# Performance work log

Measured on AMD Instinct MI355X. Metric: run time of the kernel, lower is better.

## Reference

```python
import jax, jax.numpy as jnp
import numpy as np

DIM = 2048
BATCH = 16384


def setup_inputs() -> dict:
    key = jax.random.key(0)
    k_x, k_h, k_w, k_b, k_d = jax.random.split(key, 5)
    x = jax.random.normal(k_x, (BATCH, DIM), dtype=jnp.float32)
    h = jax.random.normal(k_h, (BATCH, DIM), dtype=jnp.float32)
    # nn.Linear(dim, dim): weight [out, in], bias [out]
    W = jax.random.normal(k_w, (DIM, DIM), dtype=jnp.float32) / np.sqrt(DIM)
    b = jax.random.normal(k_b, (DIM,), dtype=jnp.float32) * 0.01
    # nn.Parameter(torch.zeros(dim)) initialized to zeros, but use small random for nontrivial grads
    decay = jax.random.normal(k_d, (DIM,), dtype=jnp.float32) * 0.1
    return {"x": x, "h": h, "W": W, "b": b, "decay": decay}


def reference(x, h, W, b, decay):
    # alpha = sigmoid(decay); h_new = alpha * h + x @ W^T + b
    alpha = jax.nn.sigmoid(decay)  # [dim]
    h_new = alpha * h + jnp.einsum("bd,ed->be", x, W) + b  # [batch, dim]
    return (h_new, h_new)
```

## Files before the change

kernel.cpp:

```cpp
#include <hip/hip_runtime.h>
#include <hip/hip_bf16.h>

#define M_BATCH 16384
#define N_DIM   2048
#define K_DIM   2048

typedef __attribute__((ext_vector_type(8))) short bf16x8;
typedef __attribute__((ext_vector_type(4))) float f32x4;

__device__ __forceinline__ unsigned short f2bf_rne(float f) {
    union { float f; unsigned int u; } v; v.f = f;
    unsigned int r = v.u + 0x7fffu + ((v.u >> 16) & 1u);
    return (unsigned short)(r >> 16);
}

__global__ __launch_bounds__(256) void cvt_f32_bf16_x8(
        const float* __restrict__ src, unsigned short* __restrict__ dst, int n8) {
    int i = blockIdx.x * blockDim.x + threadIdx.x;
    if (i >= n8) return;
    const float4* s4 = (const float4*)src;
    float4 a = s4[2 * i];
    float4 b = s4[2 * i + 1];
    union { unsigned short h[8]; uint4 v; } r;
    r.h[0] = f2bf_rne(a.x); r.h[1] = f2bf_rne(a.y);
    r.h[2] = f2bf_rne(a.z); r.h[3] = f2bf_rne(a.w);
    r.h[4] = f2bf_rne(b.x); r.h[5] = f2bf_rne(b.y);
    r.h[6] = f2bf_rne(b.z); r.h[7] = f2bf_rne(b.w);
    ((uint4*)dst)[i] = r.v;
}

__device__ __forceinline__ void gld_lds16(const void* g, void* l) {
    __builtin_amdgcn_global_load_lds(
        (const __attribute__((address_space(1))) void*)g,
        (__attribute__((address_space(3))) void*)l, 16, 0, 0);
}

__global__ __launch_bounds__(256, 2) void lrnn_gemm_fused(
        const unsigned short* __restrict__ Xb,
        const unsigned short* __restrict__ Wb,
        const float* __restrict__ H,
        const float* __restrict__ bias,
        const float* __restrict__ decay,
        float* __restrict__ out) {
    __shared__ __align__(16) unsigned short As[128 * 32];
    __shared__ __align__(16) unsigned short Bs[128 * 32];

    const int tid  = threadIdx.x;
    const int wave = tid >> 6;
    const int lane = tid & 63;
    const int quad = lane >> 4;
    const int l16  = lane & 15;

    const int row0 = blockIdx.y * 128;
    const int col0 = blockIdx.x * 128;
    const int wm = (wave >> 1) * 64;
    const int wn = (wave & 1) * 64;

    const int t0  = wave * 64 + lane;
    const int r0s = t0 >> 2, kc0 = (t0 & 3) * 8;
    const int t1  = 256 + t0;
    const int r1s = t1 >> 2, kc1 = (t1 & 3) * 8;

    const unsigned short* gA0 = Xb + (size_t)(row0 + r0s) * K_DIM + kc0;
    const unsigned short* gA1 = Xb + (size_t)(row0 + r1s) * K_DIM + kc1;
    const unsigned short* gB0 = Wb + (size_t)(col0 + r0s) * K_DIM + kc0;
    const unsigned short* gB1 = Wb + (size_t)(col0 + r1s) * K_DIM + kc1;

    unsigned short* lA0 = As + (wave * 64) * 8;
    unsigned short* lA1 = As + (256 + wave * 64) * 8;
    unsigned short* lB0 = Bs + (wave * 64) * 8;
    unsigned short* lB1 = Bs + (256 + wave * 64) * 8;

    f32x4 acc[4][4] = {};

    for (int k0 = 0; k0 < K_DIM; k0 += 32) {
        gld_lds16(gA0 + k0, lA0);
        gld_lds16(gA1 + k0, lA1);
        gld_lds16(gB0 + k0, lB0);
        gld_lds16(gB1 + k0, lB1);
        __syncthreads();

        bf16x8 af[4], bfr[4];
#pragma unroll
        for (int i = 0; i < 4; ++i) {
            af[i]  = *(const bf16x8*)(As + (wm + i * 16 + l16) * 32 + quad * 8);
            bfr[i] = *(const bf16x8*)(Bs + (wn + i * 16 + l16) * 32 + quad * 8);
        }
#pragma unroll
        for (int i = 0; i < 4; ++i)
#pragma unroll
            for (int j = 0; j < 4; ++j)
                acc[i][j] = __builtin_amdgcn_mfma_f32_16x16x32_bf16(
                    af[i], bfr[j], acc[i][j], 0, 0, 0);
        __syncthreads();
    }

    const size_t MN = (size_t)M_BATCH * N_DIM;
#pragma unroll
    for (int j = 0; j < 4; ++j) {
        const int col = col0 + wn + j * 16 + l16;
        const float al = 1.0f / (1.0f + __expf(-decay[col]));
        const float bb = bias[col];
#pragma unroll
        for (int i = 0; i < 4; ++i) {
            const int row = row0 + wm + i * 16 + quad * 4;
#pragma unroll
            for (int r = 0; r < 4; ++r) {
                size_t idx = (size_t)(row + r) * N_DIM + col;
                float v = al * H[idx] + acc[i][j][r] + bb;
                out[idx] = v;
                out[MN + idx] = v;
            }
        }
    }
}

extern "C" void kernel_launch(void* const* d_in, const int* in_sizes, int n_in,
                              void* d_out, int out_size, void* d_ws, size_t ws_size,
                              hipStream_t stream) {
    const float* x     = (const float*)d_in[0];
    const float* h     = (const float*)d_in[1];
    const float* W     = (const float*)d_in[2];
    const float* b     = (const float*)d_in[3];
    const float* decay = (const float*)d_in[4];
    float* out = (float*)d_out;

    unsigned short* xb = (unsigned short*)d_ws;
    unsigned short* wb = xb + (size_t)M_BATCH * K_DIM;

    const int n8x = M_BATCH * K_DIM / 8;
    cvt_f32_bf16_x8<<<n8x / 256, 256, 0, stream>>>(x, xb, n8x);
    const int n8w = N_DIM * K_DIM / 8;
    cvt_f32_bf16_x8<<<n8w / 256, 256, 0, stream>>>(W, wb, n8w);

    dim3 grid(N_DIM / 128, M_BATCH / 128);
    lrnn_gemm_fused<<<grid, 256, 0, stream>>>(xb, wb, h, b, decay, out);
}
```

Baseline: 612.1 us.

## Rewrite GEMM as 256x256 tile, 8-wave, double-buffered swizzled LDS pipeline

Result: slower. 681.6 us (+11.4%).

```diff
diff --git a/kernel.cpp b/kernel.cpp
--- a/kernel.cpp
+++ b/kernel.cpp
@@ -1,5 +1,4 @@
 #include <hip/hip_runtime.h>
-#include <hip/hip_bf16.h>
 
 #define M_BATCH 16384
 #define N_DIM   2048
@@ -29,81 +28,158 @@
     ((uint4*)dst)[i] = r.v;
 }
 
-__device__ __forceinline__ void gld_lds16(const void* g, void* l) {
+__device__ __forceinline__ void gld_lds16(const unsigned short* g, unsigned short* l) {
     __builtin_amdgcn_global_load_lds(
         (const __attribute__((address_space(1))) void*)g,
         (__attribute__((address_space(3))) void*)l, 16, 0, 0);
 }
 
-__global__ __launch_bounds__(256, 2) void lrnn_gemm_fused(
+#define BAR()   __builtin_amdgcn_s_barrier()
+#define LGKM0() asm volatile("s_waitcnt lgkmcnt(0)" ::: "memory")
+#define VMC4()  asm volatile("s_waitcnt vmcnt(4)" ::: "memory")
+#define PRIO1() __builtin_amdgcn_s_setprio(1)
+#define PRIO0() __builtin_amdgcn_s_setprio(0)
+
+__global__ __launch_bounds__(512, 2) void lrnn_gemm_fused(
         const unsigned short* __restrict__ Xb,
         const unsigned short* __restrict__ Wb,
         const float* __restrict__ H,
         const float* __restrict__ bias,
         const float* __restrict__ decay,
         float* __restrict__ out) {
-    __shared__ __align__(16) unsigned short As[128 * 32];
-    __shared__ __align__(16) unsigned short Bs[128 * 32];
+    extern __shared__ char smem_raw[];
+    unsigned short* lds = (unsigned short*)smem_raw;
 
     const int tid  = threadIdx.x;
     const int wave = tid >> 6;
     const int lane = tid & 63;
-    const int quad = lane >> 4;
     const int l16  = lane & 15;
-
-    const int row0 = blockIdx.y * 128;
-    const int col0 = blockIdx.x * 128;
-    const int wm = (wave >> 1) * 64;
-    const int wn = (wave & 1) * 64;
-
-    const int t0  = wave * 64 + lane;
-    const int r0s = t0 >> 2, kc0 = (t0 & 3) * 8;
-    const int t1  = 256 + t0;
-    const int r1s = t1 >> 2, kc1 = (t1 & 3) * 8;
-
-    const unsigned short* gA0 = Xb + (size_t)(row0 + r0s) * K_DIM + kc0;
-    const unsigned short* gA1 = Xb + (size_t)(row0 + r1s) * K_DIM + kc1;
-    const unsigned short* gB0 = Wb + (size_t)(col0 + r0s) * K_DIM + kc0;
-    const unsigned short* gB1 = Wb + (size_t)(col0 + r1s) * K_DIM + kc1;
-
-    unsigned short* lA0 = As + (wave * 64) * 8;
-    unsigned short* lA1 = As + (256 + wave * 64) * 8;
-    unsigned short* lB0 = Bs + (wave * 64) * 8;
-    unsigned short* lB1 = Bs + (256 + wave * 64) * 8;
-
-    f32x4 acc[4][4] = {};
-
-    for (int k0 = 0; k0 < K_DIM; k0 += 32) {
-        gld_lds16(gA0 + k0, lA0);
-        gld_lds16(gA1 + k0, lA1);
-        gld_lds16(gB0 + k0, lB0);
-        gld_lds16(gB1 + k0, lB1);
-        __syncthreads();
-
-        bf16x8 af[4], bfr[4];
-#pragma unroll
-        for (int i = 0; i < 4; ++i) {
-            af[i]  = *(const bf16x8*)(As + (wm + i * 16 + l16) * 32 + quad * 8);
-            bfr[i] = *(const bf16x8*)(Bs + (wn + i * 16 + l16) * 32 + quad * 8);
-        }
-#pragma unroll
-        for (int i = 0; i < 4; ++i)
-#pragma unroll
-            for (int j = 0; j < 4; ++j)
-                acc[i][j] = __builtin_amdgcn_mfma_f32_16x16x32_bf16(
-                    af[i], bfr[j], acc[i][j], 0, 0, 0);
-        __syncthreads();
+    const int q    = lane >> 4;
+    const int l7   = lane & 7;
+    const int wm   = wave >> 2;
+    const int wn   = wave & 3;
+
+    const int row0 = blockIdx.y * 256;
+    const int col0 = blockIdx.x * 256;
+
+    const int r0c = tid >> 3,      s0c = (tid & 7) ^ (r0c & 7);
+    const int c1  = 512 + tid;
+    const int r1c = c1 >> 3,       s1c = (c1 & 7) ^ (r1c & 7);
+    const size_t off0 = (size_t)r0c * K_DIM + s0c * 8;
+    const size_t off1 = (size_t)r1c * K_DIM + s1c * 8;
+    const int stl0 = wave * 512;
+    const int stl1 = 4096 + wave * 512;
+
+    const unsigned short* Xg = Xb + (size_t)row0 * K_DIM;
+    const unsigned short* Wg = Wb + (size_t)col0 * K_DIM;
+    const size_t hstride = (size_t)128 * K_DIM;
+
+    int roF[4][2];
+#pragma unroll
+    for (int i_ = 0; i_ < 4; ++i_)
+#pragma unroll
+        for (int k_ = 0; k_ < 2; ++k_)
+            roF[i_][k_] = (i_ * 16 + l16) * 64 + (((q + 4 * k_) ^ l7) * 8);
+
+    const unsigned short* rdA = lds + wm * 8192;
+    const unsigned short* rdB = lds + 16384 + (wn >> 1) * 8192 + (wn & 1) * 4096;
+
+    f32x4 acc[8][4] = {};
+    bf16x8 a[4][2], b[2][2];
+
+#define STAGE_A(buf, h, t) do { \
+    unsigned short* lb_ = lds + (buf) * 32768 + (h) * 8192; \
+    const unsigned short* gs_ = Xg + (size_t)(h) * hstride + (size_t)(t) * 64; \
+    gld_lds16(gs_ + off0, lb_ + stl0); \
+    gld_lds16(gs_ + off1, lb_ + stl1); } while (0)
+
+#define STAGE_B(buf, h, t) do { \
+    unsigned short* lb_ = lds + (buf) * 32768 + 16384 + (h) * 8192; \
+    const unsigned short* gs_ = Wg + (size_t)(h) * hstride + (size_t)(t) * 64; \
+    gld_lds16(gs_ + off0, lb_ + stl0); \
+    gld_lds16(gs_ + off1, lb_ + stl1); } while (0)
+
+#define LOAD_A(buf, qi) do { \
+    const unsigned short* p_ = rdA + (buf) * 32768 + (qi) * 4096; \
+    _Pragma("unroll") for (int i_ = 0; i_ < 4; ++i_) \
+    _Pragma("unroll") for (int k_ = 0; k_ < 2; ++k_) \
+        a[i_][k_] = *(const bf16x8*)(p_ + roF[i_][k_]); } while (0)
+
+#define LOAD_B(buf, qj) do { \
+    const unsigned short* p_ = rdB + (buf) * 32768 + (qj) * 2048; \
+    _Pragma("unroll") for (int j_ = 0; j_ < 2; ++j_) \
+    _Pragma("unroll") for (int k_ = 0; k_ < 2; ++k_) \
+        b[j_][k_] = *(const bf16x8*)(p_ + roF[j_][k_]); } while (0)
+
+#define MFMA_Q(qi, qj) do { \
+    _Pragma("unroll") for (int i_ = 0; i_ < 4; ++i_) \
+    _Pragma("unroll") for (int j_ = 0; j_ < 2; ++j_) \
+    _Pragma("unroll") for (int k_ = 0; k_ < 2; ++k_) \
+        acc[(qi)*4 + i_][(qj)*2 + j_] = __builtin_amdgcn_mfma_f32_16x16x32_bf16( \
+            a[i_][k_], b[j_][k_], acc[(qi)*4 + i_][(qj)*2 + j_], 0, 0, 0); } while (0)
+
+    STAGE_A(0, 0, 0); STAGE_A(0, 1, 0); STAGE_B(0, 0, 0); STAGE_B(0, 1, 0);
+    STAGE_A(1, 0, 1); STAGE_A(1, 1, 1);
+    VMC4();
+    BAR();
+
+#pragma unroll 1
+    for (int it = 0; it < 16; ++it) {
+        const int t1 = 2 * it + 1;
+        const int u0 = (2 * it + 2) & 31;
+        const int u1 = (2 * it + 3) & 31;
+
+        LOAD_A(0, 0); LOAD_B(0, 0);
+        STAGE_B(1, 0, t1); STAGE_B(1, 1, t1);
+        BAR(); LGKM0();
+        PRIO1(); MFMA_Q(0, 0); PRIO0();
+        BAR();
+        LOAD_B(0, 1);
+        BAR(); LGKM0();
+        PRIO1(); MFMA_Q(0, 1); PRIO0();
+        BAR();
+        LOAD_A(0, 1);
+        BAR(); LGKM0();
+        PRIO1(); MFMA_Q(1, 1); PRIO0();
+        BAR();
+        LOAD_B(0, 0);
+        STAGE_A(0, 0, u0); STAGE_A(0, 1, u0);
+        VMC4();
+        BAR(); LGKM0();
+        PRIO1(); MFMA_Q(1, 0); PRIO0();
+        BAR();
+        LOAD_A(1, 0); LOAD_B(1, 0);
+        STAGE_B(0, 0, u0); STAGE_B(0, 1, u0);
+        BAR(); LGKM0();
+        PRIO1(); MFMA_Q(0, 0); PRIO0();
+        BAR();
+        LOAD_B(1, 1);
+        BAR(); LGKM0();
+        PRIO1(); MFMA_Q(0, 1); PRIO0();
+        BAR();
+        LOAD_A(1, 1);
+        BAR(); LGKM0();
+        PRIO1(); MFMA_Q(1, 1); PRIO0();
+        BAR();
+        LOAD_B(1, 0);
+        STAGE_A(1, 0, u1); STAGE_A(1, 1, u1);
+        VMC4();
+        BAR(); LGKM0();
+        PRIO1(); MFMA_Q(1, 0); PRIO0();
+        BAR();
     }
 
+    asm volatile("s_waitcnt vmcnt(0)" ::: "memory");
+
     const size_t MN = (size_t)M_BATCH * N_DIM;
 #pragma unroll
     for (int j = 0; j < 4; ++j) {
-        const int col = col0 + wn + j * 16 + l16;
+        const int col = col0 + wn * 64 + j * 16 + l16;
         const float al = 1.0f / (1.0f + __expf(-decay[col]));
         const float bb = bias[col];
 #pragma unroll
-        for (int i = 0; i < 4; ++i) {
-            const int row = row0 + wm + i * 16 + quad * 4;
+        for (int i = 0; i < 8; ++i) {
+            const int row = row0 + wm * 128 + i * 16 + q * 4;
 #pragma unroll
             for (int r = 0; r < 4; ++r) {
                 size_t idx = (size_t)(row + r) * N_DIM + col;
@@ -113,6 +189,12 @@
             }
         }
     }
+
+#undef STAGE_A
+#undef STAGE_B
+#undef LOAD_A
+#undef LOAD_B
+#undef MFMA_Q
 }
 
 extern "C" void kernel_launch(void* const* d_in, const int* in_sizes, int n_in,
@@ -128,11 +210,18 @@
     unsigned short* xb = (unsigned short*)d_ws;
     unsigned short* wb = xb + (size_t)M_BATCH * K_DIM;
 
+    static bool cfg = false;
+    if (!cfg) {
+        hipFuncSetAttribute((const void*)lrnn_gemm_fused,
+                            hipFuncAttributeMaxDynamicSharedMemorySize, 131072);
+        cfg = true;
+    }
+
     const int n8x = M_BATCH * K_DIM / 8;
     cvt_f32_bf16_x8<<<n8x / 256, 256, 0, stream>>>(x, xb, n8x);
     const int n8w = N_DIM * K_DIM / 8;
     cvt_f32_bf16_x8<<<n8w / 256, 256, 0, stream>>>(W, wb, n8w);
 
-    dim3 grid(N_DIM / 128, M_BATCH / 128);
-    lrnn_gemm_fused<<<grid, 256, 0, stream>>>(xb, wb, h, b, decay, out);
-}
+    dim3 grid(N_DIM / 256, M_BATCH / 256);
+    lrnn_gemm_fused<<<grid, 512, 131072, stream>>>(xb, wb, h, b, decay, out);
+}
```

## Double-buffer LDS with K=64 stages, XOR swizzle, and grouped tile remap

Applied to the files above, without the earlier changes.

Result: faster. 597.9 us (-2.3%).

```diff
diff --git a/kernel.cpp b/kernel.cpp
--- a/kernel.cpp
+++ b/kernel.cpp
@@ -1,5 +1,4 @@
 #include <hip/hip_runtime.h>
-#include <hip/hip_bf16.h>
 
 #define M_BATCH 16384
 #define N_DIM   2048
@@ -29,11 +28,17 @@
     ((uint4*)dst)[i] = r.v;
 }
 
-__device__ __forceinline__ void gld_lds16(const void* g, void* l) {
+__device__ __forceinline__ void gld_lds16(const unsigned short* g, unsigned short* l) {
     __builtin_amdgcn_global_load_lds(
         (const __attribute__((address_space(1))) void*)g,
         (__attribute__((address_space(3))) void*)l, 16, 0, 0);
 }
+
+#define BAR()   __builtin_amdgcn_s_barrier()
+#define LGKM0() asm volatile("s_waitcnt lgkmcnt(0)" ::: "memory")
+#define VMC0()  asm volatile("s_waitcnt vmcnt(0)" ::: "memory")
+#define PRIO1() __builtin_amdgcn_s_setprio(1)
+#define PRIO0() __builtin_amdgcn_s_setprio(0)
 
 __global__ __launch_bounds__(256, 2) void lrnn_gemm_fused(
         const unsigned short* __restrict__ Xb,
@@ -42,68 +47,104 @@
         const float* __restrict__ bias,
         const float* __restrict__ decay,
         float* __restrict__ out) {
-    __shared__ __align__(16) unsigned short As[128 * 32];
-    __shared__ __align__(16) unsigned short Bs[128 * 32];
+    __shared__ __align__(16) unsigned short lds[32768];
 
     const int tid  = threadIdx.x;
     const int wave = tid >> 6;
     const int lane = tid & 63;
-    const int quad = lane >> 4;
     const int l16  = lane & 15;
+    const int q    = lane >> 4;
+    const int l7   = lane & 7;
+    const int wr   = wave >> 1;
+    const int wc   = wave & 1;
 
-    const int row0 = blockIdx.y * 128;
-    const int col0 = blockIdx.x * 128;
-    const int wm = (wave >> 1) * 64;
-    const int wn = (wave & 1) * 64;
+    const int wid = blockIdx.y * 16 + blockIdx.x;
+    const int nid = (wid & 7) * 256 + (wid >> 3);
+    const int bx  = nid & 15;
+    const int by  = nid >> 4;
+    const int row0 = by * 128;
+    const int col0 = bx * 128;
 
-    const int t0  = wave * 64 + lane;
-    const int r0s = t0 >> 2, kc0 = (t0 & 3) * 8;
-    const int t1  = 256 + t0;
-    const int r1s = t1 >> 2, kc1 = (t1 & 3) * 8;
+    const unsigned short* gA[4];
+    const unsigned short* gB[4];
+    int ldst[4];
+#pragma unroll
+    for (int i = 0; i < 4; ++i) {
+        const int c = tid + 256 * i;
+        const int r = c >> 3;
+        const int s = (c & 7) ^ (r & 7);
+        gA[i] = Xb + (size_t)(row0 + r) * K_DIM + s * 8;
+        gB[i] = Wb + (size_t)(col0 + r) * K_DIM + s * 8;
+        ldst[i] = wave * 512 + i * 2048;
+    }
 
-    const unsigned short* gA0 = Xb + (size_t)(row0 + r0s) * K_DIM + kc0;
-    const unsigned short* gA1 = Xb + (size_t)(row0 + r1s) * K_DIM + kc1;
-    const unsigned short* gB0 = Wb + (size_t)(col0 + r0s) * K_DIM + kc0;
-    const unsigned short* gB1 = Wb + (size_t)(col0 + r1s) * K_DIM + kc1;
+    int fo[4][2];
+#pragma unroll
+    for (int i = 0; i < 4; ++i)
+#pragma unroll
+        for (int kk = 0; kk < 2; ++kk)
+            fo[i][kk] = (i * 16 + l16) * 64 + (((q + 4 * kk) ^ l7) * 8);
 
-    unsigned short* lA0 = As + (wave * 64) * 8;
-    unsigned short* lA1 = As + (256 + wave * 64) * 8;
-    unsigned short* lB0 = Bs + (wave * 64) * 8;
-    unsigned short* lB1 = Bs + (256 + wave * 64) * 8;
+    const int aBase = wr * 4096;
+    const int bBase = 16384 + wc * 4096;
 
     f32x4 acc[4][4] = {};
+    bf16x8 a[4][2], b[4][2];
 
-    for (int k0 = 0; k0 < K_DIM; k0 += 32) {
-        gld_lds16(gA0 + k0, lA0);
-        gld_lds16(gA1 + k0, lA1);
-        gld_lds16(gB0 + k0, lB0);
-        gld_lds16(gB1 + k0, lB1);
-        __syncthreads();
+#define STAGE(buf, t) do { \
+    const int k0_ = (t) * 64; \
+    unsigned short* la_ = lds + (buf) * 8192; \
+    unsigned short* lb_ = lds + 16384 + (buf) * 8192; \
+    _Pragma("unroll") for (int i_ = 0; i_ < 4; ++i_) gld_lds16(gA[i_] + k0_, la_ + ldst[i_]); \
+    _Pragma("unroll") for (int i_ = 0; i_ < 4; ++i_) gld_lds16(gB[i_] + k0_, lb_ + ldst[i_]); \
+    } while (0)
 
-        bf16x8 af[4], bfr[4];
-#pragma unroll
-        for (int i = 0; i < 4; ++i) {
-            af[i]  = *(const bf16x8*)(As + (wm + i * 16 + l16) * 32 + quad * 8);
-            bfr[i] = *(const bf16x8*)(Bs + (wn + i * 16 + l16) * 32 + quad * 8);
-        }
-#pragma unroll
-        for (int i = 0; i < 4; ++i)
-#pragma unroll
-            for (int j = 0; j < 4; ++j)
-                acc[i][j] = __builtin_amdgcn_mfma_f32_16x16x32_bf16(
-                    af[i], bfr[j], acc[i][j], 0, 0, 0);
-        __syncthreads();
+#define LOAD(buf) do { \
+    const unsigned short* pa_ = lds + (buf) * 8192 + aBase; \
+    const unsigned short* pb_ = lds + (buf) * 8192 + bBase; \
+    _Pragma("unroll") for (int i_ = 0; i_ < 4; ++i_) \
+    _Pragma("unroll") for (int k_ = 0; k_ < 2; ++k_) { \
+        a[i_][k_] = *(const bf16x8*)(pa_ + fo[i_][k_]); \
+        b[i_][k_] = *(const bf16x8*)(pb_ + fo[i_][k_]); } \
+    } while (0)
+
+#define MFMA_ALL() do { \
+    _Pragma("unroll") for (int i_ = 0; i_ < 4; ++i_) \
+    _Pragma("unroll") for (int j_ = 0; j_ < 4; ++j_) \
+    _Pragma("unroll") for (int k_ = 0; k_ < 2; ++k_) \
+        acc[i_][j_] = __builtin_amdgcn_mfma_f32_16x16x32_bf16( \
+            a[i_][k_], b[j_][k_], acc[i_][j_], 0, 0, 0); \
+    } while (0)
+
+    STAGE(0, 0);
+    VMC0();
+    BAR();
+
+#pragma unroll 1
+    for (int it = 0; it < 16; ++it) {
+        STAGE(1, 2 * it + 1);
+        LOAD(0);
+        LGKM0();
+        PRIO1(); MFMA_ALL(); PRIO0();
+        VMC0();
+        BAR();
+        if (it < 15) STAGE(0, 2 * it + 2);
+        LOAD(1);
+        LGKM0();
+        PRIO1(); MFMA_ALL(); PRIO0();
+        VMC0();
+        BAR();
     }
 
     const size_t MN = (size_t)M_BATCH * N_DIM;
 #pragma unroll
     for (int j = 0; j < 4; ++j) {
-        const int col = col0 + wn + j * 16 + l16;
+        const int col = col0 + wc * 64 + j * 16 + l16;
         const float al = 1.0f / (1.0f + __expf(-decay[col]));
         const float bb = bias[col];
 #pragma unroll
         for (int i = 0; i < 4; ++i) {
-            const int row = row0 + wm + i * 16 + quad * 4;
+            const int row = row0 + wr * 64 + i * 16 + q * 4;
 #pragma unroll
             for (int r = 0; r < 4; ++r) {
                 size_t idx = (size_t)(row + r) * N_DIM + col;
@@ -113,6 +154,10 @@
             }
         }
     }
+
+#undef STAGE
+#undef LOAD
+#undef MFMA_ALL
 }
 
 extern "C" void kernel_launch(void* const* d_in, const int* in_sizes, int n_in,
```
